# Kernel optimization log

Hardware: AMD Instinct MI355X
Metric: run time of the kernel (lower is better)

## Reference

```python
import jax, jax.numpy as jnp
import numpy as np

D_MODEL = 1024
D_STATE = 128
HEAD_DIM = 64
EXPAND = 2
K = 4  # conv_kernel
N_GROUPS = 1
D_INNER = EXPAND * D_MODEL            # 2048
N_HEADS = D_INNER // HEAD_DIM         # 32
D_PROJ = 2 * D_INNER + 2 * N_GROUPS * D_STATE + N_HEADS  # 4384
EPS = 1e-6


def _rmsnorm(x, w):
    return x * jax.lax.rsqrt(jnp.mean(x * x, axis=-1, keepdims=True) + EPS) * w


def setup_inputs() -> dict:
    key = jax.random.key(0)
    ks = jax.random.split(key, 8)
    B, L = 2, 2048
    x = jax.random.normal(ks[0], (B, L, D_MODEL), jnp.float32)
    norm_w = jnp.ones((D_MODEL,), jnp.float32)
    in_proj_w = jax.random.normal(ks[1], (D_PROJ, D_MODEL), jnp.float32) / np.sqrt(D_MODEL).astype(np.float32)
    conv_w = jax.random.normal(ks[2], (D_INNER, K), jnp.float32) / np.sqrt(K).astype(np.float32)
    conv_b = jnp.zeros((D_INNER,), jnp.float32)
    A_log = jnp.log(jax.random.uniform(ks[3], (N_HEADS,), jnp.float32) * 15.0 + 1.0)
    D = jnp.ones((N_HEADS,), jnp.float32)
    dt_bias = jnp.log(jax.random.uniform(ks[4], (N_HEADS,), jnp.float32) * 0.099 + 0.001)
    out_proj_w = jax.random.normal(ks[5], (D_MODEL, D_INNER), jnp.float32) / np.sqrt(D_INNER).astype(np.float32)
    return dict(x=x, norm_w=norm_w, in_proj_w=in_proj_w, conv_w=conv_w, conv_b=conv_b,
                A_log=A_log, D=D, dt_bias=dt_bias, out_proj_w=out_proj_w)


def reference(x, norm_w, in_proj_w, conv_w, conv_b, A_log, D, dt_bias, out_proj_w):
    batch, L, _ = x.shape
    residual = x
    xn = _rmsnorm(x, norm_w)
    proj = jnp.einsum('bld,pd->blp', xn, in_proj_w)  # (B,L,D_PROJ)

    # split fused projection -> z, x_ssm, B, C, dt_raw
    i = 0
    z = proj[:, :, i:i + D_INNER]; i += D_INNER
    x_ssm = proj[:, :, i:i + D_INNER]; i += D_INNER
    bc = N_GROUPS * D_STATE
    Bm = proj[:, :, i:i + bc].reshape(batch, L, N_GROUPS, D_STATE); i += bc
    Cm = proj[:, :, i:i + bc].reshape(batch, L, N_GROUPS, D_STATE); i += bc
    dt_raw = proj[:, :, i:i + N_HEADS]

    # causal depthwise conv1d (left-pad K-1) + SiLU
    xp = jnp.pad(x_ssm, ((0, 0), (K - 1, 0), (0, 0)))
    x_conv = conv_b
    for k in range(K):
        x_conv = x_conv + xp[:, k:k + L, :] * conv_w[:, k]
    x_conv = jax.nn.silu(x_conv)

    xh = x_conv.reshape(batch, L, N_HEADS, HEAD_DIM)
    dt = jax.nn.softplus(dt_raw + dt_bias)          # (B,L,H)
    dA = jnp.exp(-jnp.exp(A_log) * dt)              # (B,L,H)
    dtx = dt[..., None] * xh                        # (B,L,H,P)

    gidx = jnp.arange(N_HEADS) // (N_HEADS // N_GROUPS)
    Bg = Bm[:, :, gidx, :]                          # (B,L,H,N)
    Cg = Cm[:, :, gidx, :]                          # (B,L,H,N)

    def step(h, inp):
        dA_t, dtx_t, B_t, C_t = inp                 # (B,H), (B,H,P), (B,H,N), (B,H,N)
        h = h * dA_t[:, :, None, None] + dtx_t[..., None] * B_t[:, :, None, :]
        y_t = jnp.einsum('bhpn,bhn->bhp', h, C_t)
        return h, y_t

    h0 = jnp.zeros((batch, N_HEADS, HEAD_DIM, D_STATE), jnp.float32)
    xs = (jnp.swapaxes(dA, 0, 1), jnp.swapaxes(dtx, 0, 1),
          jnp.swapaxes(Bg, 0, 1), jnp.swapaxes(Cg, 0, 1))
    _, ys = jax.lax.scan(step, h0, xs)              # ys: (L,B,H,P)
    y = jnp.swapaxes(ys, 0, 1) + D[None, None, :, None] * xh

    y = y.reshape(batch, L, D_INNER) * jax.nn.silu(z)
    return residual + jnp.einsum('bli,di->bld', y, out_proj_w)
```

## Files before the change

### kernel.cpp

```cpp
#include <hip/hip_runtime.h>
#include <hip/hip_bf16.h>

#define L_SEQ 2048
#define DM 1024
#define DI 2048
#define DS 128
#define NH 32
#define HD 64
#define DPROJ 4384
#define DPAD 4480
#define NBATCH 2
#define NCH 8
#define CH 256
#define B_OFF 4096
#define C_OFF 4224
#define DT_OFF 4352
#define SWZ(row) ((((row) ^ ((row) >> 3)) & 7) << 4)

typedef unsigned short u16;
typedef __attribute__((ext_vector_type(8))) short short8;
typedef __attribute__((ext_vector_type(4))) float f32x4;

#define GLL16(g, l)                                                     \
  __builtin_amdgcn_global_load_lds(                                     \
      (const __attribute__((address_space(1))) unsigned int*)(g),       \
      (__attribute__((address_space(3))) unsigned int*)(l), 16, 0, 0)

__device__ __forceinline__ u16 f2bf(float f) {
  union { float f; unsigned u; } c; c.f = f;
  unsigned u = c.u;
  u += 0x7fffu + ((u >> 16) & 1u);
  return (u16)(u >> 16);
}
__device__ __forceinline__ float bf2f(u16 u) {
  return __uint_as_float((unsigned)u << 16);
}
__device__ __forceinline__ float siluf(float x) {
  return x / (1.0f + expf(-x));
}
__device__ __forceinline__ void store_out(u16* C, size_t o, float v) { C[o] = f2bf(v); }
__device__ __forceinline__ void store_out(float* C, size_t o, float v) { C[o] = v; }

__global__ __launch_bounds__(256) void rmsnorm_kernel(
    const float* __restrict__ x, const float* __restrict__ w,
    u16* __restrict__ xnb) {
  int m = blockIdx.x;
  int t = threadIdx.x;
  const float* row = x + (size_t)m * DM;
  float4 v = *(const float4*)(row + t * 4);
  float ss = v.x * v.x + v.y * v.y + v.z * v.z + v.w * v.w;
#pragma unroll
  for (int o = 32; o > 0; o >>= 1) ss += __shfl_xor(ss, o);
  __shared__ float sred[4];
  if ((t & 63) == 0) sred[t >> 6] = ss;
  __syncthreads();
  ss = sred[0] + sred[1] + sred[2] + sred[3];
  float rs = rsqrtf(ss * (1.0f / DM) + 1e-6f);
  float4 wv = *(const float4*)(w + t * 4);
  ushort4 o;
  o.x = f2bf(v.x * rs * wv.x);
  o.y = f2bf(v.y * rs * wv.y);
  o.z = f2bf(v.z * rs * wv.z);
  o.w = f2bf(v.w * rs * wv.w);
  *(ushort4*)(xnb + (size_t)m * DM + t * 4) = o;
}

__global__ __launch_bounds__(256) void cvt_w1_kernel(
    const float* __restrict__ w, u16* __restrict__ o) {
  int r = blockIdx.x;
  int c = threadIdx.x * 4;
  ushort4 u;
  if (r < DPROJ) {
    float4 v = *(const float4*)(w + (size_t)r * DM + c);
    u.x = f2bf(v.x); u.y = f2bf(v.y); u.z = f2bf(v.z); u.w = f2bf(v.w);
  } else {
    u.x = 0; u.y = 0; u.z = 0; u.w = 0;
  }
  *(ushort4*)(o + (size_t)r * DM + c) = u;
}

__global__ __launch_bounds__(256) void cvt_w2_kernel(
    const float* __restrict__ w, u16* __restrict__ o) {
  size_t i = ((size_t)blockIdx.x * 256 + threadIdx.x) * 8;
  float4 v0 = *(const float4*)(w + i);
  float4 v1 = *(const float4*)(w + i + 4);
  ushort4 a, b;
  a.x = f2bf(v0.x); a.y = f2bf(v0.y); a.z = f2bf(v0.z); a.w = f2bf(v0.w);
  b.x = f2bf(v1.x); b.y = f2bf(v1.y); b.z = f2bf(v1.z); b.w = f2bf(v1.w);
  *(ushort4*)(o + i) = a;
  *(ushort4*)(o + i + 4) = b;
}

template <typename OT, bool RES, bool DTS>
__global__ __launch_bounds__(256, 4) void gemm_bt(
    const u16* __restrict__ A, const u16* __restrict__ Bw,
    OT* __restrict__ C, const float* __restrict__ resid,
    float* __restrict__ dts, int M, int N, int K, int nbx) {
  __shared__ u16 lA[128 * 32];
  __shared__ u16 lB[128 * 32];
  const int tid = threadIdx.x;
  const int wv = tid >> 6, lane = tid & 63;
  const int wm = wv >> 1, wn = wv & 1;

  const int nwg = gridDim.x;
  const int cpx = nwg >> 3;
  const int wg = blockIdx.x;
  const int swz = (wg & 7) * cpx + (wg >> 3);
  const int m0 = (swz / nbx) * 128, n0 = (swz % nbx) * 128;

  const int rowS = tid >> 2;
  const int colS = (tid & 3) * 8;
  const u16* gA0 = A + (size_t)(m0 + rowS) * K + colS;
  const u16* gA1 = A + (size_t)(m0 + rowS + 64) * K + colS;
  const u16* gB0 = Bw + (size_t)(n0 + rowS) * K + colS;
  const u16* gB1 = Bw + (size_t)(n0 + rowS + 64) * K + colS;

  u16* ldsA0 = lA + wv * 512;
  u16* ldsA1 = lA + 2048 + wv * 512;
  u16* ldsB0 = lB + wv * 512;
  u16* ldsB1 = lB + 2048 + wv * 512;

  f32x4 acc[4][4] = {};

  const int nk = K >> 5;
  for (int kt = 0; kt < nk; ++kt) {
    const int ko = kt << 5;
    __syncthreads();
    GLL16(gA0 + ko, ldsA0);
    GLL16(gA1 + ko, ldsA1);
    GLL16(gB0 + ko, ldsB0);
    GLL16(gB1 + ko, ldsB1);
    __syncthreads();
    short8 af[4], bfr[4];
    const int r = lane & 15;
    const int koff = (lane >> 4) * 8;
#pragma unroll
    for (int i = 0; i < 4; ++i)
      af[i] = *(const short8*)&lA[(wm * 64 + i * 16 + r) * 32 + koff];
#pragma unroll
    for (int j = 0; j < 4; ++j)
      bfr[j] = *(const short8*)&lB[(wn * 64 + j * 16 + r) * 32 + koff];
#pragma unroll
    for (int i = 0; i < 4; ++i)
#pragma unroll
      for (int j = 0; j < 4; ++j)
        acc[i][j] = __builtin_amdgcn_mfma_f32_16x16x32_bf16(
            af[i], bfr[j], acc[i][j], 0, 0, 0);
  }

  const int rbase = m0 + wm * 64 + (lane >> 4) * 4;
  const int cbase = n0 + wn * 64 + (lane & 15);
#pragma unroll
  for (int i = 0; i < 4; ++i) {
#pragma unroll
    for (int j = 0; j < 4; ++j) {
      int row0 = rbase + i * 16;
      int col = cbase + j * 16;
#pragma unroll
      for (int rr = 0; rr < 4; ++rr) {
        size_t o = (size_t)(row0 + rr) * N + col;
        float v = acc[i][j][rr];
        if (RES) v += resid[o];
        store_out(C, o, v);
        if (DTS) {
          if (col >= DT_OFF && col < DT_OFF + NH)
            dts[(size_t)(row0 + rr) * NH + (col - DT_OFF)] = v;
        }
      }
    }
  }
}

__global__ __launch_bounds__(256) void conv_kernel(
    const u16* __restrict__ proj, const float* __restrict__ cw,
    const float* __restrict__ cb, u16* __restrict__ xh) {
  int m = blockIdx.x;
  int l = m & (L_SEQ - 1);
  int c0 = threadIdx.x * 8;
  float4 wv[8];
#pragma unroll
  for (int j = 0; j < 8; ++j) wv[j] = *(const float4*)(cw + (size_t)(c0 + j) * 4);
  float acc[8];
#pragma unroll
  for (int j = 0; j < 8; ++j) acc[j] = cb[c0 + j];
#pragma unroll
  for (int k = 0; k < 4; ++k) {
    int lk = l + k - 3;
    if (lk >= 0) {
      short8 rv8 = *(const short8*)(proj + (size_t)(m + k - 3) * DPAD + DI + c0);
#pragma unroll
      for (int j = 0; j < 8; ++j) {
        float wk = (k == 0) ? wv[j].x : (k == 1) ? wv[j].y : (k == 2) ? wv[j].z : wv[j].w;
        acc[j] = fmaf(bf2f((u16)rv8[j]), wk, acc[j]);
      }
    }
  }
  short8 o;
#pragma unroll
  for (int j = 0; j < 8; ++j) o[j] = (short)f2bf(siluf(acc[j]));
  *(short8*)(xh + (size_t)m * DI + c0) = o;
}

__global__ __launch_bounds__(256) void dtda_kernel(
    const float* __restrict__ dts, const float* __restrict__ dt_bias,
    const float* __restrict__ A_log, float* __restrict__ dAdt) {
  int idx = blockIdx.x * 256 + threadIdx.x;
  int h = idx & 31;
  float raw = dts[idx] + dt_bias[h];
  float dt = fmaxf(raw, 0.0f) + log1pf(expf(-fabsf(raw)));
  float a = -expf(A_log[h]) * dt;
  float2 o; o.x = a; o.y = dt;
  *(float2*)(dAdt + (size_t)idx * 2) = o;
}


__global__ __launch_bounds__(512) void scan_state_mfma(
    const u16* __restrict__ proj, const float* __restrict__ dAdt,
    const u16* __restrict__ xhy, float* __restrict__ S,
    float* __restrict__ P) {
  __shared__ u16 sBT[128 * 64];
  __shared__ u16 sXT[64 * 64];
  __shared__ u16 sXW[64 * 64];
  __shared__ float sDt[64], sCum[64], sWs[64], sLam[64];

  const int bid = blockIdx.x;
  const int ch = bid & 7, hh = (bid >> 3) & 31, b = bid >> 8;
  const int tid = threadIdx.x;
  const int w = tid >> 6, l = tid & 63;
  const int tw = w >> 1, half = w & 1;
  const int klane = (l >> 4) * 16;
  const size_t mchunk = (size_t)(b * L_SEQ + ch * CH);

  f32x4 hAcc[4] = {};
  float ctot = 0.0f;

  auto STAGE = [&](int sc) {
    const size_t m0 = mchunk + (size_t)sc * 64;
    {
      const int tp = tid >> 4;
      const int n0 = (tid & 15) * 8;
      const u16* r0 = proj + (m0 + 2 * tp) * DPAD + B_OFF + n0;
      short8 lo8 = *(const short8*)r0;
      short8 hi8 = *(const short8*)(r0 + DPAD);
#pragma unroll
      for (int q = 0; q < 8; ++q) {
        int n = n0 + q;
        unsigned v = (unsigned)(u16)lo8[q] | ((unsigned)(u16)hi8[q] << 16);
        *(unsigned*)((char*)sBT + ((n * 128 + 4 * tp) ^ SWZ(n))) = v;
      }
    }
    {
      const int sx = tid >> 3;
      const int p0 = (tid & 7) * 8;
      short8 xv8 = *(const short8*)(xhy + (m0 + sx) * DI + hh * 64 + p0);
#pragma unroll
      for (int i = 0; i < 8; ++i) {
        int p = p0 + i;
        *(u16*)((char*)sXT + ((p * 128 + 2 * sx) ^ SWZ(p))) = (u16)xv8[i];
      }
    }
    if (tid < 64) {
      float2 ad = *(const float2*)(dAdt + (m0 + tid) * 64 + hh * 2);
      float a = ad.x, dtv = ad.y;
      sDt[tid] = dtv;
      float val = a;
#pragma unroll
      for (int o = 1; o < 64; o <<= 1) {
        float t2 = __shfl_up(val, o);
        if (tid >= o) val += t2;
      }
      sCum[tid] = val;
      float c63 = __shfl(val, 63);
      sWs[tid] = __expf(c63 - val) * dtv;
      sLam[tid] = __expf(val);
    }
  };

  STAGE(0);
  __syncthreads();

  for (int sc = 0; sc < 4; ++sc) {
    {
      int p = tid >> 3, sg = tid & 7;
      int byteX = (p * 128 + sg * 16) ^ SWZ(p);
      short8 xv = *(short8*)((char*)sXT + byteX);
      short8 outp;
#pragma unroll
      for (int j = 0; j < 8; ++j)
        outp[j] = (short)f2bf(bf2f((u16)xv[j]) * sWs[sg * 8 + j]);
      *(short8*)((char*)sXW + byteX) = outp;
    }
    __syncthreads();

    {
      float lam63 = sLam[63];
      ctot += sCum[63];
#pragma unroll
      for (int j = 0; j < 4; ++j) {
        hAcc[j][0] *= lam63; hAcc[j][1] *= lam63;
        hAcc[j][2] *= lam63; hAcc[j][3] *= lam63;
      }
      int prow = tw * 16 + (l & 15);
      short8 aXW[2];
#pragma unroll
      for (int kk = 0; kk < 2; ++kk)
        aXW[kk] = *(short8*)((char*)sXW + ((prow * 128 + kk * 64 + klane) ^ SWZ(prow)));
#pragma unroll
      for (int j = 0; j < 4; ++j) {
        int nrow = (half * 4 + j) * 16 + (l & 15);
#pragma unroll
        for (int kk = 0; kk < 2; ++kk) {
          short8 bBT = *(short8*)((char*)sBT + ((nrow * 128 + kk * 64 + klane) ^ SWZ(nrow)));
          hAcc[j] = __builtin_amdgcn_mfma_f32_16x16x32_bf16(aXW[kk], bBT, hAcc[j], 0, 0, 0);
        }
      }
    }
    __syncthreads();
    if (sc < 3) STAGE(sc + 1);
    __syncthreads();
  }

  float* Sb = S + (size_t)((b * 32 + hh) * NCH + ch) * 8192;
  const int p0 = tw * 16 + (l >> 4) * 4;
#pragma unroll
  for (int j = 0; j < 4; ++j) {
    int n = (half * 4 + j) * 16 + (l & 15);
#pragma unroll
    for (int r = 0; r < 4; ++r)
      Sb[(p0 + r) * 128 + n] = hAcc[j][r];
  }
  if (tid == 0) P[(b * 32 + hh) * NCH + ch] = __expf(ctot);
}

__global__ __launch_bounds__(256) void combine_kernel(
    float* __restrict__ S, const float* __restrict__ P) {
  int tid = blockIdx.x * 256 + threadIdx.x;
  int bh = tid >> 13, pn = tid & 8191;
  size_t base = (size_t)bh * NCH * 8192 + pn;
  float E = 0.0f;
#pragma unroll
  for (int c = 0; c < NCH; ++c) {
    size_t o = base + (size_t)c * 8192;
    float Sc = S[o];
    S[o] = E;
    E = fmaf(P[bh * NCH + c], E, Sc);
  }
}

__global__ __launch_bounds__(512) void scan_y_mfma(
    const u16* __restrict__ proj, const float* __restrict__ dAdt,
    const u16* __restrict__ xhy, const float* __restrict__ Dv,
    const float* __restrict__ S, u16* __restrict__ yb) {
  __shared__ u16 sC[64 * 128];
  __shared__ u16 sB[64 * 128];
  __shared__ u16 sHb[64 * 128];
  __shared__ u16 sBT[128 * 64];
  __shared__ u16 sXT[64 * 64];
  __shared__ u16 sXW[64 * 64];
  __shared__ u16 sW[64 * 64];
  __shared__ float sDt[64], sCum[64], sWs[64], sLam[64];

  const int bid = blockIdx.x;
  const int ch = bid & 7, hh = (bid >> 3) & 31, b = bid >> 8;
  const int tid = threadIdx.x;
  const int w = tid >> 6, l = tid & 63;
  const int tw = w >> 1, half = w & 1;
  const int klane = (l >> 4) * 16;
  const float Dh = Dv[hh];
  const size_t mchunk = (size_t)(b * L_SEQ + ch * CH);

  f32x4 hAcc[4];
  {
    const float* Sb = S + (size_t)((b * 32 + hh) * NCH + ch) * 8192;
    const int p0 = tw * 16 + (l >> 4) * 4;
#pragma unroll
    for (int j = 0; j < 4; ++j) {
      int n = (half * 4 + j) * 16 + (l & 15);
#pragma unroll
      for (int r = 0; r < 4; ++r)
        hAcc[j][r] = Sb[(p0 + r) * 128 + n];
    }
    int p = tid >> 3, sg = tid & 7;
#pragma unroll
    for (int i = 0; i < 4; ++i) {
      float4 v = *(const float4*)(Sb + p * 128 + sg * 16 + 4 * i);
      ushort4 u;
      u.x = f2bf(v.x); u.y = f2bf(v.y); u.z = f2bf(v.z); u.w = f2bf(v.w);
      *(ushort4*)((char*)sHb + ((p * 256 + (sg * 16 + 4 * i) * 2) ^ SWZ(p))) = u;
    }
  }

  auto STAGE = [&](int sc) {
    const size_t m0 = mchunk + (size_t)sc * 64;
    {
      const int tp = tid >> 4;
      const int n0 = (tid & 15) * 8;
      const u16* r0 = proj + (m0 + 2 * tp) * DPAD;
      short8 b0 = *(const short8*)(r0 + B_OFF + n0);
      short8 b1 = *(const short8*)(r0 + DPAD + B_OFF + n0);
      short8 c0v = *(const short8*)(r0 + C_OFF + n0);
      short8 c1v = *(const short8*)(r0 + DPAD + C_OFF + n0);
      *(short8*)((char*)sB + ((2 * tp * 256 + n0 * 2) ^ SWZ(2 * tp))) = b0;
      *(short8*)((char*)sB + (((2 * tp + 1) * 256 + n0 * 2) ^ SWZ(2 * tp + 1))) = b1;
      *(short8*)((char*)sC + ((2 * tp * 256 + n0 * 2) ^ SWZ(2 * tp))) = c0v;
      *(short8*)((char*)sC + (((2 * tp + 1) * 256 + n0 * 2) ^ SWZ(2 * tp + 1))) = c1v;
#pragma unroll
      for (int q = 0; q < 8; ++q) {
        int n = n0 + q;
        unsigned v = (unsigned)(u16)b0[q] | ((unsigned)(u16)b1[q] << 16);
        *(unsigned*)((char*)sBT + ((n * 128 + 4 * tp) ^ SWZ(n))) = v;
      }
    }
    {
      const int sx = tid >> 3;
      const int p0 = (tid & 7) * 8;
      short8 xv8 = *(const short8*)(xhy + (m0 + sx) * DI + hh * 64 + p0);
#pragma unroll
      for (int i = 0; i < 8; ++i) {
        int p = p0 + i;
        *(u16*)((char*)sXT + ((p * 128 + 2 * sx) ^ SWZ(p))) = (u16)xv8[i];
      }
    }
    if (tid < 64) {
      float2 ad = *(const float2*)(dAdt + (m0 + tid) * 64 + hh * 2);
      float a = ad.x, dtv = ad.y;
      sDt[tid] = dtv;
      float val = a;
#pragma unroll
      for (int o = 1; o < 64; o <<= 1) {
        float t2 = __shfl_up(val, o);
        if (tid >= o) val += t2;
      }
      sCum[tid] = val;
      float c63 = __shfl(val, 63);
      sWs[tid] = __expf(c63 - val) * dtv;
      sLam[tid] = __expf(val);
    }
  };

  STAGE(0);
  __syncthreads();

  for (int sc = 0; sc < 4; ++sc) {
    const size_t m0 = mchunk + (size_t)sc * 64;
    {
      int p = tid >> 3, sg = tid & 7;
      int byteX = (p * 128 + sg * 16) ^ SWZ(p);
      short8 xv = *(short8*)((char*)sXT + byteX);
      short8 outp;
#pragma unroll
      for (int j = 0; j < 8; ++j)
        outp[j] = (short)f2bf(bf2f((u16)xv[j]) * sWs[sg * 8 + j]);
      *(short8*)((char*)sXW + byteX) = outp;
    }
    __syncthreads();

    const int trow = tw * 16 + (l & 15);
    short8 aC[4];
#pragma unroll
    for (int kk = 0; kk < 4; ++kk)
      aC[kk] = *(short8*)((char*)sC + ((trow * 256 + kk * 64 + klane) ^ SWZ(trow)));

    {
      f32x4 g[2] = {};
#pragma unroll
      for (int sv2 = 0; sv2 < 2; ++sv2) {
        int srow = (half * 2 + sv2) * 16 + (l & 15);
#pragma unroll
        for (int kk = 0; kk < 4; ++kk) {
          short8 bB = *(short8*)((char*)sB + ((srow * 256 + kk * 64 + klane) ^ SWZ(srow)));
          g[sv2] = __builtin_amdgcn_mfma_f32_16x16x32_bf16(aC[kk], bB, g[sv2], 0, 0, 0);
        }
      }
#pragma unroll
      for (int sv2 = 0; sv2 < 2; ++sv2) {
        int s = (half * 2 + sv2) * 16 + (l & 15);
        float dts_ = sDt[s], cums = sCum[s];
#pragma unroll
        for (int r = 0; r < 4; ++r) {
          int t = tw * 16 + (l >> 4) * 4 + r;
          float v = (t >= s) ? g[sv2][r] * __expf(sCum[t] - cums) * dts_ : 0.0f;
          *(u16*)((char*)sW + ((t * 128 + 2 * s) ^ SWZ(t))) = f2bf(v);
        }
      }
    }
    __syncthreads();

    f32x4 y1[2] = {}, y2[2] = {};
    float lamv[4], lam63 = sLam[63];
#pragma unroll
    for (int r = 0; r < 4; ++r) lamv[r] = sLam[tw * 16 + (l >> 4) * 4 + r];
    {
      short8 aW[2];
#pragma unroll
      for (int kk = 0; kk < 2; ++kk)
        aW[kk] = *(short8*)((char*)sW + ((trow * 128 + kk * 64 + klane) ^ SWZ(trow)));
#pragma unroll
      for (int pv2 = 0; pv2 < 2; ++pv2) {
        int prow = (half * 2 + pv2) * 16 + (l & 15);
#pragma unroll
        for (int kk = 0; kk < 2; ++kk) {
          short8 bX = *(short8*)((char*)sXT + ((prow * 128 + kk * 64 + klane) ^ SWZ(prow)));
          y1[pv2] = __builtin_amdgcn_mfma_f32_16x16x32_bf16(aW[kk], bX, y1[pv2], 0, 0, 0);
        }
#pragma unroll
        for (int kk = 0; kk < 4; ++kk) {
          short8 bH = *(short8*)((char*)sHb + ((prow * 256 + kk * 64 + klane) ^ SWZ(prow)));
          y2[pv2] = __builtin_amdgcn_mfma_f32_16x16x32_bf16(aC[kk], bH, y2[pv2], 0, 0, 0);
        }
      }
#pragma unroll
      for (int j = 0; j < 4; ++j) {
        hAcc[j][0] *= lam63; hAcc[j][1] *= lam63;
        hAcc[j][2] *= lam63; hAcc[j][3] *= lam63;
      }
      short8 aXW[2];
#pragma unroll
      for (int kk = 0; kk < 2; ++kk)
        aXW[kk] = *(short8*)((char*)sXW + ((trow * 128 + kk * 64 + klane) ^ SWZ(trow)));
#pragma unroll
      for (int j = 0; j < 4; ++j) {
        int nrow = (half * 4 + j) * 16 + (l & 15);
#pragma unroll
        for (int kk = 0; kk < 2; ++kk) {
          short8 bBT = *(short8*)((char*)sBT + ((nrow * 128 + kk * 64 + klane) ^ SWZ(nrow)));
          hAcc[j] = __builtin_amdgcn_mfma_f32_16x16x32_bf16(aXW[kk], bBT, hAcc[j], 0, 0, 0);
        }
      }
    }
    __syncthreads();

    {
#pragma unroll
      for (int j = 0; j < 4; ++j) {
        int n = (half * 4 + j) * 16 + (l & 15);
#pragma unroll
        for (int r = 0; r < 4; ++r) {
          int p = tw * 16 + (l >> 4) * 4 + r;
          *(u16*)((char*)sHb + ((p * 256 + 2 * n) ^ SWZ(p))) = f2bf(hAcc[j][r]);
        }
      }
#pragma unroll
      for (int pv2 = 0; pv2 < 2; ++pv2) {
        int p = (half * 2 + pv2) * 16 + (l & 15);
#pragma unroll
        for (int r = 0; r < 4; ++r) {
          int t = tw * 16 + (l >> 4) * 4 + r;
          int col = hh * 64 + p;
          size_t gy = (m0 + t) * DI + col;
          float xv = bf2f(xhy[gy]);
          float yv = y1[pv2][r] + lamv[r] * y2[pv2][r] + Dh * xv;
          float zv = bf2f(proj[(m0 + t) * DPAD + col]);
          yb[gy] = f2bf(yv * siluf(zv));
        }
      }
      if (sc < 3) STAGE(sc + 1);
    }
    __syncthreads();
  }
}

extern "C" void kernel_launch(void* const* d_in, const int* in_sizes, int n_in,
                              void* d_out, int out_size, void* d_ws, size_t ws_size,
                              hipStream_t stream) {
  const float* x      = (const float*)d_in[0];
  const float* norm_w = (const float*)d_in[1];
  const float* w1     = (const float*)d_in[2];
  const float* cw     = (const float*)d_in[3];
  const float* cb     = (const float*)d_in[4];
  const float* A_log  = (const float*)d_in[5];
  const float* Dv     = (const float*)d_in[6];
  const float* dt_b   = (const float*)d_in[7];
  const float* w2     = (const float*)d_in[8];
  float* out = (float*)d_out;

  char* ws = (char*)d_ws;
  u16*   xnb  = (u16*)(ws);
  u16*   w1b  = (u16*)(ws + 8388608);
  u16*   w2b  = (u16*)(ws + 17563648);
  u16*   proj = (u16*)(ws + 21757952);
  float* dts  = (float*)(ws + 58458112);
  u16*   xhy  = (u16*)(ws + 58982400);
  float* dAdt = (float*)(ws + 75759616);
  u16*   yb   = (u16*)(ws + 76808192);
  float* S    = (float*)(ws + 93585408);
  float* P    = (float*)(ws + 110362624);

  const int M = NBATCH * L_SEQ;

  rmsnorm_kernel<<<M, 256, 0, stream>>>(x, norm_w, xnb);
  cvt_w1_kernel<<<DPAD, 256, 0, stream>>>(w1, w1b);
  cvt_w2_kernel<<<1024, 256, 0, stream>>>(w2, w2b);
  gemm_bt<u16, false, true><<<(DPAD / 128) * (M / 128), 256, 0, stream>>>(
      xnb, w1b, proj, nullptr, dts, M, DPAD, DM, DPAD / 128);
  conv_kernel<<<M, 256, 0, stream>>>(proj, cw, cb, xhy);
  dtda_kernel<<<M * NH / 256, 256, 0, stream>>>(dts, dt_b, A_log, dAdt);
  scan_state_mfma<<<512, 512, 0, stream>>>(proj, dAdt, xhy, S, P);
  combine_kernel<<<2048, 256, 0, stream>>>(S, P);
  scan_y_mfma<<<512, 512, 0, stream>>>(proj, dAdt, xhy, Dv, S, yb);
  gemm_bt<float, true, false><<<(DM / 128) * (M / 128), 256, 0, stream>>>(
      yb, w2b, out, x, nullptr, M, DM, DI, DM / 128);
}
```

Before: 216.0 us.

## Double-buffer GEMM LDS tiles and use narrower N tile for out-projection

The bf16 MFMA GEMM now double-buffers its A and B LDS tiles. The global-to-LDS load for the next K step is issued before computing on the current buffer, and synchronisation uses explicit vmcnt waits and barriers instead of two __syncthreads per iteration. The kernel is templated on the N tile width, and the out-projection GEMM uses a 64-wide tile, doubling its workgroup count for better CU occupancy. This costs twice the LDS per block. The loop also assumes an even number of K steps.

```diff
diff --git a/kernel.cpp b/kernel.cpp
--- a/kernel.cpp
+++ b/kernel.cpp
@@ -25,6 +25,9 @@
   __builtin_amdgcn_global_load_lds(                                     \
       (const __attribute__((address_space(1))) unsigned int*)(g),       \
       (__attribute__((address_space(3))) unsigned int*)(l), 16, 0, 0)
+#define VMCNT0 asm volatile("s_waitcnt vmcnt(0)" ::: "memory")
+#define SBAR __builtin_amdgcn_s_barrier()
+#define SGB0 __builtin_amdgcn_sched_barrier(0)
 
 __device__ __forceinline__ u16 f2bf(float f) {
   union { float f; unsigned u; } c; c.f = f;
@@ -91,13 +94,15 @@
   *(ushort4*)(o + i + 4) = b;
 }
 
-template <typename OT, bool RES, bool DTS>
+template <typename OT, bool RES, bool DTS, int BN>
 __global__ __launch_bounds__(256, 4) void gemm_bt(
     const u16* __restrict__ A, const u16* __restrict__ Bw,
     OT* __restrict__ C, const float* __restrict__ resid,
     float* __restrict__ dts, int M, int N, int K, int nbx) {
-  __shared__ u16 lA[128 * 32];
-  __shared__ u16 lB[128 * 32];
+  constexpr int WN = BN / 2;
+  constexpr int NJ = WN / 16;
+  __shared__ u16 lA[2][128 * 32];
+  __shared__ u16 lB[2][BN * 32];
   const int tid = threadIdx.x;
   const int wv = tid >> 6, lane = tid & 63;
   const int wm = wv >> 1, wn = wv & 1;
@@ -106,54 +111,67 @@
   const int cpx = nwg >> 3;
   const int wg = blockIdx.x;
   const int swz = (wg & 7) * cpx + (wg >> 3);
-  const int m0 = (swz / nbx) * 128, n0 = (swz % nbx) * 128;
+  const int m0 = (swz / nbx) * 128, n0 = (swz % nbx) * BN;
 
   const int rowS = tid >> 2;
   const int colS = (tid & 3) * 8;
   const u16* gA0 = A + (size_t)(m0 + rowS) * K + colS;
   const u16* gA1 = A + (size_t)(m0 + rowS + 64) * K + colS;
   const u16* gB0 = Bw + (size_t)(n0 + rowS) * K + colS;
-  const u16* gB1 = Bw + (size_t)(n0 + rowS + 64) * K + colS;
-
-  u16* ldsA0 = lA + wv * 512;
-  u16* ldsA1 = lA + 2048 + wv * 512;
-  u16* ldsB0 = lB + wv * 512;
-  u16* ldsB1 = lB + 2048 + wv * 512;
-
-  f32x4 acc[4][4] = {};
-
-  const int nk = K >> 5;
-  for (int kt = 0; kt < nk; ++kt) {
+  const u16* gB1 = Bw + (size_t)(n0 + ((BN == 128) ? rowS + 64 : rowS)) * K + colS;
+
+  auto stage = [&](int kt, int buf) {
     const int ko = kt << 5;
-    __syncthreads();
-    GLL16(gA0 + ko, ldsA0);
-    GLL16(gA1 + ko, ldsA1);
-    GLL16(gB0 + ko, ldsB0);
-    GLL16(gB1 + ko, ldsB1);
-    __syncthreads();
-    short8 af[4], bfr[4];
-    const int r = lane & 15;
-    const int koff = (lane >> 4) * 8;
+    GLL16(gA0 + ko, &lA[buf][wv * 512]);
+    GLL16(gA1 + ko, &lA[buf][2048 + wv * 512]);
+    GLL16(gB0 + ko, &lB[buf][wv * 512]);
+    if (BN == 128) GLL16(gB1 + ko, &lB[buf][2048 + wv * 512]);
+  };
+
+  f32x4 acc[4][NJ] = {};
+  const int r = lane & 15;
+  const int koff = (lane >> 4) * 8;
+
+  auto compute = [&](int buf) {
+    short8 af[4], bfr[NJ];
 #pragma unroll
     for (int i = 0; i < 4; ++i)
-      af[i] = *(const short8*)&lA[(wm * 64 + i * 16 + r) * 32 + koff];
-#pragma unroll
-    for (int j = 0; j < 4; ++j)
-      bfr[j] = *(const short8*)&lB[(wn * 64 + j * 16 + r) * 32 + koff];
+      af[i] = *(const short8*)&lA[buf][(wm * 64 + i * 16 + r) * 32 + koff];
+#pragma unroll
+    for (int j = 0; j < NJ; ++j)
+      bfr[j] = *(const short8*)&lB[buf][(wn * WN + j * 16 + r) * 32 + koff];
 #pragma unroll
     for (int i = 0; i < 4; ++i)
 #pragma unroll
-      for (int j = 0; j < 4; ++j)
+      for (int j = 0; j < NJ; ++j)
         acc[i][j] = __builtin_amdgcn_mfma_f32_16x16x32_bf16(
             af[i], bfr[j], acc[i][j], 0, 0, 0);
+  };
+
+  const int nk = K >> 5;
+  stage(0, 0);
+  VMCNT0;
+  SBAR;
+  SGB0;
+  for (int kt = 0; kt < nk; kt += 2) {
+    stage(kt + 1, 1);
+    compute(0);
+    VMCNT0;
+    SBAR;
+    SGB0;
+    if (kt + 2 < nk) stage(kt + 2, 0);
+    compute(1);
+    VMCNT0;
+    SBAR;
+    SGB0;
   }
 
   const int rbase = m0 + wm * 64 + (lane >> 4) * 4;
-  const int cbase = n0 + wn * 64 + (lane & 15);
+  const int cbase = n0 + wn * WN + (lane & 15);
 #pragma unroll
   for (int i = 0; i < 4; ++i) {
 #pragma unroll
-    for (int j = 0; j < 4; ++j) {
+    for (int j = 0; j < NJ; ++j) {
       int row0 = rbase + i * 16;
       int col = cbase + j * 16;
 #pragma unroll
@@ -591,13 +609,13 @@
   rmsnorm_kernel<<<M, 256, 0, stream>>>(x, norm_w, xnb);
   cvt_w1_kernel<<<DPAD, 256, 0, stream>>>(w1, w1b);
   cvt_w2_kernel<<<1024, 256, 0, stream>>>(w2, w2b);
-  gemm_bt<u16, false, true><<<(DPAD / 128) * (M / 128), 256, 0, stream>>>(
+  gemm_bt<u16, false, true, 128><<<(DPAD / 128) * (M / 128), 256, 0, stream>>>(
       xnb, w1b, proj, nullptr, dts, M, DPAD, DM, DPAD / 128);
   conv_kernel<<<M, 256, 0, stream>>>(proj, cw, cb, xhy);
   dtda_kernel<<<M * NH / 256, 256, 0, stream>>>(dts, dt_b, A_log, dAdt);
   scan_state_mfma<<<512, 512, 0, stream>>>(proj, dAdt, xhy, S, P);
   combine_kernel<<<2048, 256, 0, stream>>>(S, P);
   scan_y_mfma<<<512, 512, 0, stream>>>(proj, dAdt, xhy, Dv, S, yb);
-  gemm_bt<float, true, false><<<(DM / 128) * (M / 128), 256, 0, stream>>>(
-      yb, w2b, out, x, nullptr, M, DM, DI, DM / 128);
-}
+  gemm_bt<float, true, false, 64><<<(DM / 64) * (M / 128), 256, 0, stream>>>(
+      yb, w2b, out, x, nullptr, M, DM, DI, DM / 64);
+}
```

Result: faster. 210.1 us (-2.7%).
